# Optimization experiments

Measured on AMD Instinct MI355X. Metric: run time of the kernel, lower is better.

## Reference

```python
import jax, jax.numpy as jnp
import numpy as np

N_NODES = 100000
N_EDGES = 1600000
DIM = 64
LAYERS = 2


def setup_inputs() -> dict:
    key = jax.random.key(0)
    k1, k2, k3, k4 = jax.random.split(key, 4)
    h = jax.random.normal(k1, (N_NODES, DIM), dtype=jnp.float32)
    w = jax.random.uniform(k2, (N_EDGES,), dtype=jnp.float32)
    src = jax.random.randint(k3, (N_EDGES,), 0, N_NODES, dtype=jnp.int32)
    dst = jax.random.randint(k4, (N_EDGES,), 0, N_NODES, dtype=jnp.int32)
    return {"h": h, "w": w, "src": src, "dst": dst}


def reference(h, w, src, dst):
    N = h.shape[0]
    # weighted in-degree, clamped at 1 (DGL in_degrees(weight='w').clamp(min=1))
    deg = jnp.maximum(jax.ops.segment_sum(w, dst, num_segments=N), 1.0)
    norm = deg[:, None] ** -0.5  # [N, 1]
    embs = [h]
    for _ in range(LAYERS):
        h_norm = h * norm                              # [N, d]
        m = h_norm[src] * w[:, None]                   # [E, d] edge messages (u_mul_e)
        neigh_sum = jax.ops.segment_sum(m, dst, num_segments=N)  # fn.sum
        h = neigh_sum * norm
        embs.append(h)
    # mean over [h0, h1, ..., hL]
    return jnp.mean(jnp.stack(embs, axis=1), axis=1)
```

## Files before the change

kernel.cpp:

```cpp
#include <hip/hip_runtime.h>
#include <hip/hip_bf16.h>

#define D 64
#define THREADS 256
#define BKT_BITS 9
#define BKT_NODES (1 << BKT_BITS)
#define CHUNK 8192

__device__ __forceinline__ unsigned f2bf(float f) {
    unsigned u = __float_as_uint(f);
    return (u + 0x7fffu + ((u >> 16) & 1u)) >> 16;
}
__device__ __forceinline__ float2 bfpair(unsigned v) {
    return make_float2(__uint_as_float(v << 16), __uint_as_float(v & 0xffff0000u));
}

__global__ void p1a_hist(const int* __restrict__ dst, int* __restrict__ blockCount,
                         int E, int B) {
    __shared__ int lc[256];
    int t = threadIdx.x;
    lc[t] = 0;
    __syncthreads();
    int base = blockIdx.x * CHUNK;
    int end = min(base + CHUNK, E);
    for (int e = base + t; e < end; e += THREADS)
        atomicAdd(&lc[dst[e] >> BKT_BITS], 1);
    __syncthreads();
    if (t < B) blockCount[(long long)blockIdx.x * B + t] = lc[t];
}

__global__ void p1b_scanblocks(int* __restrict__ blockCount, int* __restrict__ total,
                               int NBLK, int B) {
    __shared__ int sm[256];
    int b = blockIdx.x, t = threadIdx.x;
    int run = 0;
    for (int base = 0; base < NBLK; base += 256) {
        int i = base + t;
        int v = (i < NBLK) ? blockCount[(long long)i * B + b] : 0;
        sm[t] = v;
        __syncthreads();
        for (int off = 1; off < 256; off <<= 1) {
            int u = (t >= off) ? sm[t - off] : 0;
            __syncthreads();
            sm[t] += u;
            __syncthreads();
        }
        if (i < NBLK) blockCount[(long long)i * B + b] = run + sm[t] - v;
        run += sm[255];
        __syncthreads();
    }
    if (t == 0) total[b] = run;
}

__global__ void p1c_scanbuckets(const int* __restrict__ total, int* __restrict__ bstart,
                                int B, int E) {
    __shared__ int sm[256];
    int t = threadIdx.x;
    int run = 0;
    for (int base = 0; base < B; base += 256) {
        int i = base + t;
        int v = (i < B) ? total[i] : 0;
        sm[t] = v;
        __syncthreads();
        for (int off = 1; off < 256; off <<= 1) {
            int u = (t >= off) ? sm[t - off] : 0;
            __syncthreads();
            sm[t] += u;
            __syncthreads();
        }
        if (i < B) bstart[i] = run + sm[t] - v;
        run += sm[255];
        __syncthreads();
    }
    if (t == 0) bstart[B] = E;
}

__global__ void p1d_scatter(const int* __restrict__ dst, const int* __restrict__ src,
                            const float* __restrict__ w, const int* __restrict__ blockCount,
                            const int* __restrict__ bstart, int2* __restrict__ temp,
                            int E, int B) {
    __shared__ int cur[256];
    int t = threadIdx.x;
    if (t < B) cur[t] = bstart[t] + blockCount[(long long)blockIdx.x * B + t];
    __syncthreads();
    int base = blockIdx.x * CHUNK;
    int end = min(base + CHUNK, E);
    for (int e = base + t; e < end; e += THREADS) {
        int d = dst[e];
        int b = d >> BKT_BITS;
        int pos = atomicAdd(&cur[b], 1);
        temp[pos] = make_int2(src[e] | ((d & (BKT_NODES - 1)) << 17),
                              __float_as_int(w[e]));
    }
}

__global__ void p2a_norm(const int2* __restrict__ temp, const int* __restrict__ bstart,
                         int* __restrict__ rowptr, float* __restrict__ norm,
                         int N, int E, int B) {
    __shared__ int cnt[BKT_NODES];
    __shared__ float degs[BKT_NODES];
    __shared__ int sm[256];
    int b = blockIdx.x, t = threadIdx.x;
    int ebeg = bstart[b], eend = bstart[b + 1];
    for (int i = t; i < BKT_NODES; i += THREADS) { cnt[i] = 0; degs[i] = 0.0f; }
    __syncthreads();
    for (int e = ebeg + t; e < eend; e += THREADS) {
        int2 pk = temp[e];
        int dl = (pk.x >> 17) & (BKT_NODES - 1);
        atomicAdd(&cnt[dl], 1);
        atomicAdd(&degs[dl], __int_as_float(pk.y));
    }
    __syncthreads();
    int run = 0;
    for (int base = 0; base < BKT_NODES; base += 256) {
        int v = cnt[base + t];
        sm[t] = v;
        __syncthreads();
        for (int off = 1; off < 256; off <<= 1) {
            int u = (t >= off) ? sm[t - off] : 0;
            __syncthreads();
            sm[t] += u;
            __syncthreads();
        }
        cnt[base + t] = run + sm[t] - v;
        run += sm[255];
        __syncthreads();
    }
    int node0 = b << BKT_BITS;
    for (int i = t; i < BKT_NODES; i += THREADS) {
        int node = node0 + i;
        if (node < N) {
            rowptr[node] = ebeg + cnt[i];
            norm[node] = rsqrtf(fmaxf(degs[i], 1.0f));
        }
    }
    if (b == 0 && t == 0) rowptr[N] = E;
}

__global__ void p2b_place(const int2* __restrict__ temp, const int* __restrict__ bstart,
                          const int* __restrict__ rowptr, const float* __restrict__ norm,
                          int2* __restrict__ packed, int N, int E, int B) {
    __shared__ int cur[BKT_NODES];
    int b = blockIdx.x, t = threadIdx.x;
    int ebeg = bstart[b], eend = bstart[b + 1];
    int node0 = b << BKT_BITS;
    for (int i = t; i < BKT_NODES; i += THREADS) {
        int node = node0 + i;
        cur[i] = (node < N) ? rowptr[node] : E;
    }
    __syncthreads();
    for (int e = ebeg + t; e < eend; e += THREADS) {
        int2 pk = temp[e];
        int dl = (pk.x >> 17) & (BKT_NODES - 1);
        int s = pk.x & 0x1ffff;
        int pos = atomicAdd(&cur[dl], 1);
        float c = __int_as_float(pk.y) * norm[s];
        packed[pos] = make_int2(s, __float_as_int(c));
    }
}

__global__ void tobf16_kernel(const float* __restrict__ h, unsigned* __restrict__ hbf2,
                              long long nd4) {
    long long i = (long long)blockIdx.x * blockDim.x + threadIdx.x;
    if (i < nd4) {
        float4 v = ((const float4*)h)[i];
        ((uint2*)hbf2)[i] = make_uint2(f2bf(v.x) | (f2bf(v.y) << 16),
                                       f2bf(v.z) | (f2bf(v.w) << 16));
    }
}

__global__ void gather1_kernel(const uint2* __restrict__ h_in, const int2* __restrict__ packed,
                               const int* __restrict__ rowptr, const float* __restrict__ norm,
                               uint2* __restrict__ h_out, int N) {
    int node = blockIdx.x * (blockDim.x >> 4) + (threadIdx.x >> 4);
    int lane = threadIdx.x & 15;
    if (node >= N) return;
    int j = rowptr[node], end = rowptr[node + 1];
    float a00 = 0, a01 = 0, a02 = 0, a03 = 0;
    float a10 = 0, a11 = 0, a12 = 0, a13 = 0;
    float a20 = 0, a21 = 0, a22 = 0, a23 = 0;
    float a30 = 0, a31 = 0, a32 = 0, a33 = 0;
    for (; j + 4 <= end; j += 4) {
        int2 p0 = packed[j], p1 = packed[j + 1], p2 = packed[j + 2], p3 = packed[j + 3];
        uint2 r0 = h_in[((long long)p0.x << 4) + lane];
        uint2 r1 = h_in[((long long)p1.x << 4) + lane];
        uint2 r2 = h_in[((long long)p2.x << 4) + lane];
        uint2 r3 = h_in[((long long)p3.x << 4) + lane];
        float c0 = __int_as_float(p0.y);
        float c1 = __int_as_float(p1.y);
        float c2 = __int_as_float(p2.y);
        float c3 = __int_as_float(p3.y);
        float2 f0a = bfpair(r0.x), f0b = bfpair(r0.y);
        float2 f1a = bfpair(r1.x), f1b = bfpair(r1.y);
        float2 f2a = bfpair(r2.x), f2b = bfpair(r2.y);
        float2 f3a = bfpair(r3.x), f3b = bfpair(r3.y);
        a00 = fmaf(f0a.x, c0, a00); a01 = fmaf(f0a.y, c0, a01);
        a02 = fmaf(f0b.x, c0, a02); a03 = fmaf(f0b.y, c0, a03);
        a10 = fmaf(f1a.x, c1, a10); a11 = fmaf(f1a.y, c1, a11);
        a12 = fmaf(f1b.x, c1, a12); a13 = fmaf(f1b.y, c1, a13);
        a20 = fmaf(f2a.x, c2, a20); a21 = fmaf(f2a.y, c2, a21);
        a22 = fmaf(f2b.x, c2, a22); a23 = fmaf(f2b.y, c2, a23);
        a30 = fmaf(f3a.x, c3, a30); a31 = fmaf(f3a.y, c3, a31);
        a32 = fmaf(f3b.x, c3, a32); a33 = fmaf(f3b.y, c3, a33);
    }
    for (; j < end; ++j) {
        int2 p = packed[j];
        uint2 r = h_in[((long long)p.x << 4) + lane];
        float c = __int_as_float(p.y);
        float2 fa = bfpair(r.x), fb = bfpair(r.y);
        a00 = fmaf(fa.x, c, a00); a01 = fmaf(fa.y, c, a01);
        a02 = fmaf(fb.x, c, a02); a03 = fmaf(fb.y, c, a03);
    }
    float nv = norm[node];
    float d0 = ((a00 + a10) + (a20 + a30)) * nv;
    float d1 = ((a01 + a11) + (a21 + a31)) * nv;
    float d2 = ((a02 + a12) + (a22 + a32)) * nv;
    float d3 = ((a03 + a13) + (a23 + a33)) * nv;
    h_out[((long long)node << 4) + lane] =
        make_uint2(f2bf(d0) | (f2bf(d1) << 16), f2bf(d2) | (f2bf(d3) << 16));
}

__global__ void gather2_final_kernel(const uint2* __restrict__ h0bf, const uint2* __restrict__ h1bf,
                                     const int2* __restrict__ packed, const int* __restrict__ rowptr,
                                     const float* __restrict__ norm, float* __restrict__ out, int N) {
    int node = blockIdx.x * (blockDim.x >> 4) + (threadIdx.x >> 4);
    int lane = threadIdx.x & 15;
    if (node >= N) return;
    int j = rowptr[node], end = rowptr[node + 1];
    float a00 = 0, a01 = 0, a02 = 0, a03 = 0;
    float a10 = 0, a11 = 0, a12 = 0, a13 = 0;
    float a20 = 0, a21 = 0, a22 = 0, a23 = 0;
    float a30 = 0, a31 = 0, a32 = 0, a33 = 0;
    for (; j + 4 <= end; j += 4) {
        int2 p0 = packed[j], p1 = packed[j + 1], p2 = packed[j + 2], p3 = packed[j + 3];
        uint2 r0 = h1bf[((long long)p0.x << 4) + lane];
        uint2 r1 = h1bf[((long long)p1.x << 4) + lane];
        uint2 r2 = h1bf[((long long)p2.x << 4) + lane];
        uint2 r3 = h1bf[((long long)p3.x << 4) + lane];
        float c0 = __int_as_float(p0.y);
        float c1 = __int_as_float(p1.y);
        float c2 = __int_as_float(p2.y);
        float c3 = __int_as_float(p3.y);
        float2 f0a = bfpair(r0.x), f0b = bfpair(r0.y);
        float2 f1a = bfpair(r1.x), f1b = bfpair(r1.y);
        float2 f2a = bfpair(r2.x), f2b = bfpair(r2.y);
        float2 f3a = bfpair(r3.x), f3b = bfpair(r3.y);
        a00 = fmaf(f0a.x, c0, a00); a01 = fmaf(f0a.y, c0, a01);
        a02 = fmaf(f0b.x, c0, a02); a03 = fmaf(f0b.y, c0, a03);
        a10 = fmaf(f1a.x, c1, a10); a11 = fmaf(f1a.y, c1, a11);
        a12 = fmaf(f1b.x, c1, a12); a13 = fmaf(f1b.y, c1, a13);
        a20 = fmaf(f2a.x, c2, a20); a21 = fmaf(f2a.y, c2, a21);
        a22 = fmaf(f2b.x, c2, a22); a23 = fmaf(f2b.y, c2, a23);
        a30 = fmaf(f3a.x, c3, a30); a31 = fmaf(f3a.y, c3, a31);
        a32 = fmaf(f3b.x, c3, a32); a33 = fmaf(f3b.y, c3, a33);
    }
    for (; j < end; ++j) {
        int2 p = packed[j];
        uint2 r = h1bf[((long long)p.x << 4) + lane];
        float c = __int_as_float(p.y);
        float2 fa = bfpair(r.x), fb = bfpair(r.y);
        a00 = fmaf(fa.x, c, a00); a01 = fmaf(fa.y, c, a01);
        a02 = fmaf(fb.x, c, a02); a03 = fmaf(fb.y, c, a03);
    }
    long long idx = ((long long)node << 4) + lane;
    float nv = norm[node];
    uint2 h0r = h0bf[idx], h1r = h1bf[idx];
    float2 h0a = bfpair(h0r.x), h0b = bfpair(h0r.y);
    float2 h1a = bfpair(h1r.x), h1b = bfpair(h1r.y);
    float4 o;
    o.x = (h0a.x + h1a.x + ((a00 + a10) + (a20 + a30)) * nv) * (1.0f / 3.0f);
    o.y = (h0a.y + h1a.y + ((a01 + a11) + (a21 + a31)) * nv) * (1.0f / 3.0f);
    o.z = (h0b.x + h1b.x + ((a02 + a12) + (a22 + a32)) * nv) * (1.0f / 3.0f);
    o.w = (h0b.y + h1b.y + ((a03 + a13) + (a23 + a33)) * nv) * (1.0f / 3.0f);
    ((float4*)out)[idx] = o;
}

extern "C" void kernel_launch(void* const* d_in, const int* in_sizes, int n_in,
                              void* d_out, int out_size, void* d_ws, size_t ws_size,
                              hipStream_t stream) {
    const float* h   = (const float*)d_in[0];
    const float* w   = (const float*)d_in[1];
    const int*   src = (const int*)d_in[2];
    const int*   dst = (const int*)d_in[3];
    const int N = in_sizes[0] / D;
    const int E = in_sizes[1];
    float* out = (float*)d_out;

    const int B = (N + BKT_NODES - 1) >> BKT_BITS;
    const int NBLK = (E + CHUNK - 1) / CHUNK;

    char* ws = (char*)d_ws;
    size_t off = 0;
    auto alloc = [&](size_t bytes, size_t align) -> char* {
        off = (off + align - 1) & ~(align - 1);
        char* p = ws + off;
        off += bytes;
        return p;
    };
    float* norm     = (float*)alloc((size_t)N * 4, 16);
    int*   rowptr   = (int*)  alloc((size_t)(N + 1) * 4, 16);
    int*   total    = (int*)  alloc((size_t)B * 4, 16);
    int*   bstart   = (int*)  alloc((size_t)(B + 1) * 4, 16);
    int*   blockCnt = (int*)  alloc((size_t)NBLK * B * 4, 16);
    int2*  packed   = (int2*) alloc((size_t)E * 8, 16);
    char*  shared_region = alloc((size_t)E * 8, 128);
    int2*     temp = (int2*)shared_region;
    unsigned* h1bf = (unsigned*)shared_region;
    unsigned* h0bf = (unsigned*)alloc((size_t)N * D * 2, 128);

    const int nodes_per_block = THREADS / 16;
    const int gather_blocks = (N + nodes_per_block - 1) / nodes_per_block;
    const long long nd4 = (long long)N * D / 4;
    const int cvt_blocks = (int)((nd4 + THREADS - 1) / THREADS);

    p1a_hist<<<NBLK, THREADS, 0, stream>>>(dst, blockCnt, E, B);
    p1b_scanblocks<<<B, 256, 0, stream>>>(blockCnt, total, NBLK, B);
    p1c_scanbuckets<<<1, 256, 0, stream>>>(total, bstart, B, E);
    p1d_scatter<<<NBLK, THREADS, 0, stream>>>(dst, src, w, blockCnt, bstart, temp, E, B);
    p2a_norm<<<B, 256, 0, stream>>>(temp, bstart, rowptr, norm, N, E, B);
    p2b_place<<<B, 256, 0, stream>>>(temp, bstart, rowptr, norm, packed, N, E, B);

    tobf16_kernel<<<cvt_blocks, THREADS, 0, stream>>>(h, h0bf, nd4);

    gather1_kernel<<<gather_blocks, THREADS, 0, stream>>>((const uint2*)h0bf, packed, rowptr,
                                                          norm, (uint2*)h1bf, N);
    gather2_final_kernel<<<gather_blocks, THREADS, 0, stream>>>((const uint2*)h0bf, (const uint2*)h1bf,
                                                                packed, rowptr, norm, out, N);
}
```

Before: 234.8 us.

## Fuse CSR build phases into one persistent kernel with grid barriers

Replaces the six CSR-building kernels and the bf16 conversion kernel with a single cooperative-style kernel. Phases are separated by a software grid barrier built on global atomics, and extra blocks do the bf16 conversion alongside the histogram phase. The aim is to remove launch gaps and tail idle time between the small phases. The barrier relies on all NBLK+196 blocks being co-resident; with about 196+196 blocks this likely fits on the GPU, but it is not guaranteed, and the spin-waits add latency.

```diff
diff --git a/kernel.cpp b/kernel.cpp
--- a/kernel.cpp
+++ b/kernel.cpp
@@ -15,157 +15,163 @@
     return make_float2(__uint_as_float(v << 16), __uint_as_float(v & 0xffff0000u));
 }
 
-__global__ void p1a_hist(const int* __restrict__ dst, int* __restrict__ blockCount,
-                         int E, int B) {
-    __shared__ int lc[256];
-    int t = threadIdx.x;
-    lc[t] = 0;
+__device__ __forceinline__ void gsync(int* cnt, int* gen, int nblk) {
     __syncthreads();
-    int base = blockIdx.x * CHUNK;
-    int end = min(base + CHUNK, E);
-    for (int e = base + t; e < end; e += THREADS)
-        atomicAdd(&lc[dst[e] >> BKT_BITS], 1);
+    if (threadIdx.x == 0) {
+        int g = __hip_atomic_load(gen, __ATOMIC_RELAXED, __HIP_MEMORY_SCOPE_AGENT);
+        __threadfence();
+        int a = __hip_atomic_fetch_add(cnt, 1, __ATOMIC_ACQ_REL, __HIP_MEMORY_SCOPE_AGENT);
+        if (a == nblk - 1) {
+            __hip_atomic_store(cnt, 0, __ATOMIC_RELAXED, __HIP_MEMORY_SCOPE_AGENT);
+            __hip_atomic_fetch_add(gen, 1, __ATOMIC_ACQ_REL, __HIP_MEMORY_SCOPE_AGENT);
+        } else {
+            while (__hip_atomic_load(gen, __ATOMIC_ACQUIRE, __HIP_MEMORY_SCOPE_AGENT) == g)
+                __builtin_amdgcn_s_sleep(1);
+        }
+        __threadfence();
+    }
     __syncthreads();
-    if (t < B) blockCount[(long long)blockIdx.x * B + t] = lc[t];
-}
-
-__global__ void p1b_scanblocks(int* __restrict__ blockCount, int* __restrict__ total,
-                               int NBLK, int B) {
-    __shared__ int sm[256];
-    int b = blockIdx.x, t = threadIdx.x;
-    int run = 0;
-    for (int base = 0; base < NBLK; base += 256) {
-        int i = base + t;
-        int v = (i < NBLK) ? blockCount[(long long)i * B + b] : 0;
-        sm[t] = v;
-        __syncthreads();
-        for (int off = 1; off < 256; off <<= 1) {
-            int u = (t >= off) ? sm[t - off] : 0;
-            __syncthreads();
-            sm[t] += u;
-            __syncthreads();
-        }
-        if (i < NBLK) blockCount[(long long)i * B + b] = run + sm[t] - v;
-        run += sm[255];
-        __syncthreads();
-    }
-    if (t == 0) total[b] = run;
-}
-
-__global__ void p1c_scanbuckets(const int* __restrict__ total, int* __restrict__ bstart,
-                                int B, int E) {
-    __shared__ int sm[256];
-    int t = threadIdx.x;
-    int run = 0;
-    for (int base = 0; base < B; base += 256) {
-        int i = base + t;
-        int v = (i < B) ? total[i] : 0;
-        sm[t] = v;
-        __syncthreads();
-        for (int off = 1; off < 256; off <<= 1) {
-            int u = (t >= off) ? sm[t - off] : 0;
-            __syncthreads();
-            sm[t] += u;
-            __syncthreads();
-        }
-        if (i < B) bstart[i] = run + sm[t] - v;
-        run += sm[255];
-        __syncthreads();
-    }
-    if (t == 0) bstart[B] = E;
-}
-
-__global__ void p1d_scatter(const int* __restrict__ dst, const int* __restrict__ src,
-                            const float* __restrict__ w, const int* __restrict__ blockCount,
-                            const int* __restrict__ bstart, int2* __restrict__ temp,
-                            int E, int B) {
-    __shared__ int cur[256];
-    int t = threadIdx.x;
-    if (t < B) cur[t] = bstart[t] + blockCount[(long long)blockIdx.x * B + t];
-    __syncthreads();
-    int base = blockIdx.x * CHUNK;
-    int end = min(base + CHUNK, E);
-    for (int e = base + t; e < end; e += THREADS) {
-        int d = dst[e];
-        int b = d >> BKT_BITS;
-        int pos = atomicAdd(&cur[b], 1);
-        temp[pos] = make_int2(src[e] | ((d & (BKT_NODES - 1)) << 17),
-                              __float_as_int(w[e]));
-    }
-}
-
-__global__ void p2a_norm(const int2* __restrict__ temp, const int* __restrict__ bstart,
-                         int* __restrict__ rowptr, float* __restrict__ norm,
-                         int N, int E, int B) {
-    __shared__ int cnt[BKT_NODES];
-    __shared__ float degs[BKT_NODES];
-    __shared__ int sm[256];
-    int b = blockIdx.x, t = threadIdx.x;
-    int ebeg = bstart[b], eend = bstart[b + 1];
-    for (int i = t; i < BKT_NODES; i += THREADS) { cnt[i] = 0; degs[i] = 0.0f; }
-    __syncthreads();
-    for (int e = ebeg + t; e < eend; e += THREADS) {
-        int2 pk = temp[e];
-        int dl = (pk.x >> 17) & (BKT_NODES - 1);
-        atomicAdd(&cnt[dl], 1);
-        atomicAdd(&degs[dl], __int_as_float(pk.y));
-    }
-    __syncthreads();
-    int run = 0;
-    for (int base = 0; base < BKT_NODES; base += 256) {
-        int v = cnt[base + t];
-        sm[t] = v;
-        __syncthreads();
-        for (int off = 1; off < 256; off <<= 1) {
-            int u = (t >= off) ? sm[t - off] : 0;
-            __syncthreads();
-            sm[t] += u;
-            __syncthreads();
-        }
-        cnt[base + t] = run + sm[t] - v;
-        run += sm[255];
-        __syncthreads();
-    }
-    int node0 = b << BKT_BITS;
-    for (int i = t; i < BKT_NODES; i += THREADS) {
-        int node = node0 + i;
-        if (node < N) {
-            rowptr[node] = ebeg + cnt[i];
-            norm[node] = rsqrtf(fmaxf(degs[i], 1.0f));
-        }
-    }
-    if (b == 0 && t == 0) rowptr[N] = E;
-}
-
-__global__ void p2b_place(const int2* __restrict__ temp, const int* __restrict__ bstart,
-                          const int* __restrict__ rowptr, const float* __restrict__ norm,
-                          int2* __restrict__ packed, int N, int E, int B) {
-    __shared__ int cur[BKT_NODES];
-    int b = blockIdx.x, t = threadIdx.x;
-    int ebeg = bstart[b], eend = bstart[b + 1];
-    int node0 = b << BKT_BITS;
-    for (int i = t; i < BKT_NODES; i += THREADS) {
-        int node = node0 + i;
-        cur[i] = (node < N) ? rowptr[node] : E;
-    }
-    __syncthreads();
-    for (int e = ebeg + t; e < eend; e += THREADS) {
-        int2 pk = temp[e];
-        int dl = (pk.x >> 17) & (BKT_NODES - 1);
-        int s = pk.x & 0x1ffff;
-        int pos = atomicAdd(&cur[dl], 1);
-        float c = __int_as_float(pk.y) * norm[s];
-        packed[pos] = make_int2(s, __float_as_int(c));
-    }
-}
-
-__global__ void tobf16_kernel(const float* __restrict__ h, unsigned* __restrict__ hbf2,
-                              long long nd4) {
-    long long i = (long long)blockIdx.x * blockDim.x + threadIdx.x;
-    if (i < nd4) {
-        float4 v = ((const float4*)h)[i];
-        ((uint2*)hbf2)[i] = make_uint2(f2bf(v.x) | (f2bf(v.y) << 16),
-                                       f2bf(v.z) | (f2bf(v.w) << 16));
+}
+
+__global__ __launch_bounds__(256)
+void build_kernel(const float* __restrict__ h, const float* __restrict__ w,
+                  const int* __restrict__ src, const int* __restrict__ dst,
+                  int* __restrict__ blockCnt, int* __restrict__ total,
+                  int* __restrict__ bstart, int2* __restrict__ temp,
+                  int2* __restrict__ packed, int* __restrict__ rowptr,
+                  float* __restrict__ norm, unsigned* __restrict__ h0bf,
+                  int* __restrict__ bar,
+                  int N, int E, int B, int NBLK, long long nd4) {
+    __shared__ int   lds_i[BKT_NODES];
+    __shared__ float lds_f[BKT_NODES];
+    __shared__ int   sm[256];
+    int* cnt = bar;
+    int* gen = bar + 1;
+    const int blk = blockIdx.x, t = threadIdx.x;
+    const int TOTB = NBLK + 196;
+
+    if (blk < NBLK) {
+        lds_i[t] = 0;
+        __syncthreads();
+        int base = blk * CHUNK, end = min(base + CHUNK, E);
+        for (int e = base + t; e < end; e += THREADS)
+            atomicAdd(&lds_i[dst[e] >> BKT_BITS], 1);
+        __syncthreads();
+        if (t < B) blockCnt[(long long)blk * B + t] = lds_i[t];
+    } else {
+        long long i0 = (long long)(blk - NBLK) * THREADS + t;
+        for (long long i = i0; i < nd4; i += (long long)196 * THREADS) {
+            float4 v = ((const float4*)h)[i];
+            ((uint2*)h0bf)[i] = make_uint2(f2bf(v.x) | (f2bf(v.y) << 16),
+                                           f2bf(v.z) | (f2bf(v.w) << 16));
+        }
+    }
+    gsync(cnt, gen, TOTB);
+
+    if (blk < B) {
+        int run = 0;
+        for (int base = 0; base < NBLK; base += 256) {
+            int i = base + t;
+            int v = (i < NBLK) ? blockCnt[(long long)i * B + blk] : 0;
+            sm[t] = v;
+            __syncthreads();
+            for (int off = 1; off < 256; off <<= 1) {
+                int u = (t >= off) ? sm[t - off] : 0;
+                __syncthreads();
+                sm[t] += u;
+                __syncthreads();
+            }
+            if (i < NBLK) blockCnt[(long long)i * B + blk] = run + sm[t] - v;
+            run += sm[255];
+            __syncthreads();
+        }
+        if (t == 0) total[blk] = run;
+    }
+    gsync(cnt, gen, TOTB);
+
+    if (blk == 0) {
+        int run = 0;
+        for (int base = 0; base < B; base += 256) {
+            int i = base + t;
+            int v = (i < B) ? total[i] : 0;
+            sm[t] = v;
+            __syncthreads();
+            for (int off = 1; off < 256; off <<= 1) {
+                int u = (t >= off) ? sm[t - off] : 0;
+                __syncthreads();
+                sm[t] += u;
+                __syncthreads();
+            }
+            if (i < B) bstart[i] = run + sm[t] - v;
+            run += sm[255];
+            __syncthreads();
+        }
+        if (t == 0) bstart[B] = E;
+    }
+    gsync(cnt, gen, TOTB);
+
+    if (blk < NBLK) {
+        if (t < B) lds_i[t] = bstart[t] + blockCnt[(long long)blk * B + t];
+        __syncthreads();
+        int base = blk * CHUNK, end = min(base + CHUNK, E);
+        for (int e = base + t; e < end; e += THREADS) {
+            int d = dst[e];
+            int b = d >> BKT_BITS;
+            int pos = atomicAdd(&lds_i[b], 1);
+            temp[pos] = make_int2(src[e] | ((d & (BKT_NODES - 1)) << 17),
+                                  __float_as_int(w[e]));
+        }
+    }
+    gsync(cnt, gen, TOTB);
+
+    int ebeg = 0, eend = 0;
+    if (blk < B) {
+        ebeg = bstart[blk]; eend = bstart[blk + 1];
+        for (int i = t; i < BKT_NODES; i += THREADS) { lds_i[i] = 0; lds_f[i] = 0.0f; }
+        __syncthreads();
+        for (int e = ebeg + t; e < eend; e += THREADS) {
+            int2 pk = temp[e];
+            int dl = (pk.x >> 17) & (BKT_NODES - 1);
+            atomicAdd(&lds_i[dl], 1);
+            atomicAdd(&lds_f[dl], __int_as_float(pk.y));
+        }
+        __syncthreads();
+        int run = 0;
+        for (int base = 0; base < BKT_NODES; base += 256) {
+            int v = lds_i[base + t];
+            sm[t] = v;
+            __syncthreads();
+            for (int off = 1; off < 256; off <<= 1) {
+                int u = (t >= off) ? sm[t - off] : 0;
+                __syncthreads();
+                sm[t] += u;
+                __syncthreads();
+            }
+            lds_i[base + t] = ebeg + run + sm[t] - v;
+            run += sm[255];
+            __syncthreads();
+        }
+        int node0 = blk << BKT_BITS;
+        for (int i = t; i < BKT_NODES; i += THREADS) {
+            int node = node0 + i;
+            if (node < N) {
+                rowptr[node] = lds_i[i];
+                norm[node] = rsqrtf(fmaxf(lds_f[i], 1.0f));
+            }
+        }
+        if (blk == 0 && t == 0) rowptr[N] = E;
+    }
+    gsync(cnt, gen, TOTB);
+
+    if (blk < B) {
+        for (int e = ebeg + t; e < eend; e += THREADS) {
+            int2 pk = temp[e];
+            int dl = (pk.x >> 17) & (BKT_NODES - 1);
+            int s = pk.x & 0x1ffff;
+            int pos = atomicAdd(&lds_i[dl], 1);
+            float c = __int_as_float(pk.y) * norm[s];
+            packed[pos] = make_int2(s, __float_as_int(c));
+        }
     }
 }
 
@@ -288,6 +294,7 @@
 
     const int B = (N + BKT_NODES - 1) >> BKT_BITS;
     const int NBLK = (E + CHUNK - 1) / CHUNK;
+    const int TOTB = NBLK + 196;
 
     char* ws = (char*)d_ws;
     size_t off = 0;
@@ -301,6 +308,7 @@
     int*   rowptr   = (int*)  alloc((size_t)(N + 1) * 4, 16);
     int*   total    = (int*)  alloc((size_t)B * 4, 16);
     int*   bstart   = (int*)  alloc((size_t)(B + 1) * 4, 16);
+    int*   bar      = (int*)  alloc(2 * 4, 16);
     int*   blockCnt = (int*)  alloc((size_t)NBLK * B * 4, 16);
     int2*  packed   = (int2*) alloc((size_t)E * 8, 16);
     char*  shared_region = alloc((size_t)E * 8, 128);
@@ -311,16 +319,12 @@
     const int nodes_per_block = THREADS / 16;
     const int gather_blocks = (N + nodes_per_block - 1) / nodes_per_block;
     const long long nd4 = (long long)N * D / 4;
-    const int cvt_blocks = (int)((nd4 + THREADS - 1) / THREADS);
-
-    p1a_hist<<<NBLK, THREADS, 0, stream>>>(dst, blockCnt, E, B);
-    p1b_scanblocks<<<B, 256, 0, stream>>>(blockCnt, total, NBLK, B);
-    p1c_scanbuckets<<<1, 256, 0, stream>>>(total, bstart, B, E);
-    p1d_scatter<<<NBLK, THREADS, 0, stream>>>(dst, src, w, blockCnt, bstart, temp, E, B);
-    p2a_norm<<<B, 256, 0, stream>>>(temp, bstart, rowptr, norm, N, E, B);
-    p2b_place<<<B, 256, 0, stream>>>(temp, bstart, rowptr, norm, packed, N, E, B);
-
-    tobf16_kernel<<<cvt_blocks, THREADS, 0, stream>>>(h, h0bf, nd4);
+
+    hipMemsetAsync(bar, 0, 8, stream);
+
+    build_kernel<<<TOTB, THREADS, 0, stream>>>(h, w, src, dst, blockCnt, total, bstart,
+                                               temp, packed, rowptr, norm, h0bf, bar,
+                                               N, E, B, NBLK, nd4);
 
     gather1_kernel<<<gather_blocks, THREADS, 0, stream>>>((const uint2*)h0bf, packed, rowptr,
                                                           norm, (uint2*)h1bf, N);
```

After: 755.2 us. 222% more time.
